# Kernel optimization log

Measured on AMD Instinct MI355X. Metric: run time of the kernel, lower is better.

Reference implementation:

```python
import jax, jax.numpy as jnp
import numpy as np

DIM = 1024
E = 8
K = 2
EPS = 1e-5

def _ln(x, g, b):
    mu = jnp.mean(x, axis=-1, keepdims=True)
    var = jnp.mean(jnp.square(x - mu), axis=-1, keepdims=True)
    return (x - mu) * jax.lax.rsqrt(var + EPS) * g + b

def setup_inputs() -> dict:
    key = jax.random.key(0)
    ks = jax.random.split(key, 8)
    H = 2 * DIM
    s_in = 1.0 / np.sqrt(DIM)
    s_h = 1.0 / np.sqrt(H)
    return {
        "x": jax.random.normal(ks[0], (2, 2048, DIM), dtype=jnp.float32),
        "gate_w": jax.random.uniform(ks[1], (DIM, E), minval=-s_in, maxval=s_in, dtype=jnp.float32),
        "w1": jax.random.uniform(ks[2], (E, DIM, H), minval=-s_in, maxval=s_in, dtype=jnp.float32),
        "b1": jax.random.uniform(ks[3], (E, H), minval=-s_in, maxval=s_in, dtype=jnp.float32),
        "ln1_g": jnp.ones((E, H), dtype=jnp.float32),
        "ln1_b": jnp.zeros((E, H), dtype=jnp.float32),
        "w2": jax.random.uniform(ks[4], (E, H, DIM), minval=-s_h, maxval=s_h, dtype=jnp.float32),
        "b2": jax.random.uniform(ks[5], (E, DIM), minval=-s_h, maxval=s_h, dtype=jnp.float32),
        "ln_g": jnp.ones((DIM,), dtype=jnp.float32),
        "ln_b": jnp.zeros((DIM,), dtype=jnp.float32),
    }

def reference(x, gate_w, w1, b1, ln1_g, ln1_b, w2, b2, ln_g, ln_b):
    shape = x.shape
    xf = x.reshape(-1, shape[-1])                      # [T, D]
    gates = jax.nn.softmax(xf @ gate_w, axis=-1)       # [T, E]
    topw, topi = jax.lax.top_k(gates, K)               # [T, K]
    topw = topw / jnp.sum(topw, axis=-1, keepdims=True)
    # combine weights per expert: [T, E]
    combine = jnp.sum(topw[:, :, None] * jax.nn.one_hot(topi, E, dtype=xf.dtype), axis=1)
    # run all experts on all tokens (vectorized grouped GEMM), combine by gate mask
    h = jnp.einsum('td,edh->teh', xf, w1) + b1          # [T, E, 2D]
    h = _ln(h, ln1_g, ln1_b)
    h = jax.nn.gelu(h, approximate=False)
    y = jnp.einsum('teh,ehd->ted', h, w2) + b2          # [T, E, D]
    out = jnp.einsum('ted,te->td', y, combine)          # [T, D]
    out = _ln(out + xf, ln_g, ln_b)
    return out.reshape(shape)
```

## Files before the change

### kernel.cpp

```cpp
#include <hip/hip_runtime.h>
#include <hip/hip_bf16.h>

#define DIMX 1024
#define HID  2048
#define NE   8
#define NT   4096
#define NPAIR 8192
#define MAXSTRIP 72

typedef __attribute__((ext_vector_type(8))) __bf16 bf16x8;
typedef __attribute__((ext_vector_type(4))) float f32x4;

__device__ inline unsigned short f2bf(float f) {
  union { float f; unsigned u; } v; v.f = f;
  unsigned r = v.u + 0x7FFFu + ((v.u >> 16) & 1u);
  return (unsigned short)(r >> 16);
}
__device__ inline float bf2f(unsigned short h) {
  union { unsigned u; float f; } v; v.u = ((unsigned)h) << 16;
  return v.f;
}

__device__ __forceinline__ void gload_lds16(const unsigned short* g, unsigned short* l) {
  __builtin_amdgcn_global_load_lds(
      (const __attribute__((address_space(1))) unsigned int*)g,
      (__attribute__((address_space(3))) unsigned int*)l, 16, 0, 0);
}

#define O_CNT   0u
#define O_TOK   1024u
#define O_TK    132096u
#define O_PW    263168u
#define O_TI    394240u
#define O_TW    427008u
#define O_POFF  459776u
#define O_SE    459904u
#define O_SR0   460416u
#define O_XBF   524288u
#define O_W1T   16777216u
#define O_W2T   50331648u
#define O_H     83886080u
#define O_Y     121634816u

__global__ __launch_bounds__(256) void k_gate_cvt(const float* __restrict__ x,
                                                  const float* __restrict__ gw,
                                                  unsigned short* __restrict__ xbf,
                                                  int* __restrict__ ti,
                                                  float* __restrict__ tw) {
  int t = blockIdx.x * 4 + (threadIdx.x >> 6);
  int lane = threadIdx.x & 63;
  const float4* xr = (const float4*)(x + (size_t)t * DIMX);
  ushort4* xo = (ushort4*)(xbf + (size_t)t * DIMX);
  float p[NE];
#pragma unroll
  for (int e = 0; e < NE; e++) p[e] = 0.f;
#pragma unroll
  for (int j = 0; j < 4; j++) {
    int idx4 = j * 64 + lane;
    float4 v = xr[idx4];
    ushort4 o; o.x = f2bf(v.x); o.y = f2bf(v.y); o.z = f2bf(v.z); o.w = f2bf(v.w);
    xo[idx4] = o;
    const float4* gp = (const float4*)(gw + (size_t)(idx4 * 4) * NE);
    float4 gA = gp[0], gB = gp[1], gC = gp[2], gD = gp[3];
    float4 gE = gp[4], gF = gp[5], gG = gp[6], gH = gp[7];
    p[0] += v.x * gA.x + v.y * gC.x + v.z * gE.x + v.w * gG.x;
    p[1] += v.x * gA.y + v.y * gC.y + v.z * gE.y + v.w * gG.y;
    p[2] += v.x * gA.z + v.y * gC.z + v.z * gE.z + v.w * gG.z;
    p[3] += v.x * gA.w + v.y * gC.w + v.z * gE.w + v.w * gG.w;
    p[4] += v.x * gB.x + v.y * gD.x + v.z * gF.x + v.w * gH.x;
    p[5] += v.x * gB.y + v.y * gD.y + v.z * gF.y + v.w * gH.y;
    p[6] += v.x * gB.z + v.y * gD.z + v.z * gF.z + v.w * gH.z;
    p[7] += v.x * gB.w + v.y * gD.w + v.z * gF.w + v.w * gH.w;
  }
#pragma unroll
  for (int e = 0; e < NE; e++)
#pragma unroll
    for (int off = 32; off > 0; off >>= 1) p[e] += __shfl_xor(p[e], off);
  if (lane == 0) {
    int ia = 0; float va = p[0];
#pragma unroll
    for (int e = 1; e < NE; e++) if (p[e] > va) { va = p[e]; ia = e; }
    int ib = -1; float vb = -3.0e38f;
#pragma unroll
    for (int e = 0; e < NE; e++) { if (e == ia) continue; if (p[e] > vb) { vb = p[e]; ib = e; } }
    float w0 = 1.f / (1.f + expf(vb - va));
    ti[t * 2] = ia;     tw[t * 2] = w0;
    ti[t * 2 + 1] = ib; tw[t * 2 + 1] = 1.f - w0;
  }
}

__global__ __launch_bounds__(512) void k_build(const int* __restrict__ ti,
                                               const float* __restrict__ tw,
                                               int* __restrict__ cnt,
                                               int* __restrict__ poffs,
                                               int* __restrict__ s_e, int* __restrict__ s_r0,
                                               int* __restrict__ ptok, int* __restrict__ ptk,
                                               float* __restrict__ pw) {
  __shared__ int sti[NPAIR];
  __shared__ int scnt[NE];
  for (int i = threadIdx.x; i < NPAIR; i += 512) sti[i] = ti[i];
  __syncthreads();
  int wid = threadIdx.x >> 6;
  int lane = threadIdx.x & 63;
  int c = 0;
  for (int p = lane; p < NPAIR; p += 64) c += (sti[p] == wid) ? 1 : 0;
#pragma unroll
  for (int off = 32; off > 0; off >>= 1) c += __shfl_xor(c, off);
  if (lane == 0) scnt[wid] = c;
  __syncthreads();
  if (threadIdx.x == 0) {
    int s = 0, pacc = 0;
    for (int e = 0; e < NE; e++) {
      cnt[e] = scnt[e];
      poffs[e] = pacc;
      int ns = (scnt[e] + 127) >> 7;
      for (int k = 0; k < ns; k++) { s_e[s] = e; s_r0[s] = k * 128; s++; }
      pacc += ns * 128;
    }
    poffs[NE] = pacc;
    for (; s < MAXSTRIP; s++) { s_e[s] = -1; s_r0[s] = 0; }
  }
  int base = 0;
  for (int p0 = 0; p0 < NPAIR; p0 += 64) {
    int p = p0 + lane;
    bool m = (sti[p] == wid);
    unsigned long long mask = __ballot(m);
    if (m) {
      int pos = base + __popcll(mask & ((1ull << lane) - 1ull));
      ptok[wid * NT + pos] = p >> 1;
      ptk[wid * NT + pos] = p;
      pw[wid * NT + pos] = tw[p];
    }
    base += __popcll(mask);
  }
}

__global__ __launch_bounds__(256) void k_transpose_cvt(const float* __restrict__ in,
                                                       unsigned short* __restrict__ out,
                                                       int R, int C) {
  __shared__ float tile[64][73];
  int e = blockIdx.z;
  const float* ip = in + (size_t)e * R * C;
  unsigned short* op = out + (size_t)e * R * C;
  int c0 = blockIdx.x * 64, r0 = blockIdx.y * 64;
  int tx = threadIdx.x & 15, ty = threadIdx.x >> 4;
#pragma unroll
  for (int i = 0; i < 4; i++) {
    int row = ty + i * 16;
    float4 v = *(const float4*)(ip + (size_t)(r0 + row) * C + c0 + tx * 4);
    tile[row][tx * 4] = v.x; tile[row][tx * 4 + 1] = v.y;
    tile[row][tx * 4 + 2] = v.z; tile[row][tx * 4 + 3] = v.w;
  }
  __syncthreads();
  int rx = threadIdx.x & 15, cy = threadIdx.x >> 4;
  int r_off = rx * 4;
#pragma unroll
  for (int i = 0; i < 4; i++) {
    int cc = cy + i * 16;
    ushort4 h;
    h.x = f2bf(tile[r_off][cc]);     h.y = f2bf(tile[r_off + 1][cc]);
    h.z = f2bf(tile[r_off + 2][cc]); h.w = f2bf(tile[r_off + 3][cc]);
    *(ushort4*)(op + (size_t)(c0 + cc) * R + r0 + r_off) = h;
  }
}

#define BM 128
#define BN 128
#define BK 32

__global__ __launch_bounds__(256) void k_gemm1(
    const unsigned short* __restrict__ xbf,
    const unsigned short* __restrict__ w1t,
    const float* __restrict__ bias1,
    const int* __restrict__ cnt, const int* __restrict__ s_e,
    const int* __restrict__ s_r0, const int* __restrict__ poffs,
    const int* __restrict__ ptok,
    unsigned short* __restrict__ hpre)
{
  int s = blockIdx.y;
  int e = s_e[s];
  if (e < 0) return;
  int r0e = s_r0[s];
  int n_e = cnt[e];
  int pbase = poffs[e];
  int col0 = blockIdx.x * BN;

  __shared__ __align__(16) unsigned short As[BM][BK];
  __shared__ __align__(16) unsigned short Bs[BN][BK];

  int tid = threadIdx.x;
  int lane = tid & 63, wid = tid >> 6;
  int wr = wid >> 1, wc = wid & 1;
  int quad = lane >> 4, m16 = lane & 15;

  int i4 = lane >> 2, kc = lane & 3;
  int ga0 = r0e + wid * 32 + i4;      if (ga0 >= n_e) ga0 = n_e - 1;
  int ga1 = r0e + wid * 32 + 16 + i4; if (ga1 >= n_e) ga1 = n_e - 1;
  int t0 = ptok[e * NT + ga0];
  int t1 = ptok[e * NT + ga1];
  const unsigned short* a0p = xbf + (size_t)t0 * DIMX + kc * 8;
  const unsigned short* a1p = xbf + (size_t)t1 * DIMX + kc * 8;
  const unsigned short* bb = w1t + (size_t)e * HID * DIMX;
  const unsigned short* b0p = bb + (size_t)(col0 + wid * 32 + i4) * DIMX + kc * 8;
  const unsigned short* b1p = bb + (size_t)(col0 + wid * 32 + 16 + i4) * DIMX + kc * 8;
  unsigned short* lA0 = &As[wid * 32][0];
  unsigned short* lA1 = &As[wid * 32 + 16][0];
  unsigned short* lB0 = &Bs[wid * 32][0];
  unsigned short* lB1 = &Bs[wid * 32 + 16][0];

  f32x4 acc[4][4];
#pragma unroll
  for (int i = 0; i < 4; i++)
#pragma unroll
    for (int j = 0; j < 4; j++) acc[i][j] = (f32x4)(0.f);

  for (int k0 = 0; k0 < DIMX; k0 += BK) {
    __syncthreads();
    gload_lds16(a0p + k0, lA0);
    gload_lds16(a1p + k0, lA1);
    gload_lds16(b0p + k0, lB0);
    gload_lds16(b1p + k0, lB1);
    __syncthreads();
    bf16x8 af[4], bfr[4];
#pragma unroll
    for (int i = 0; i < 4; i++) af[i]  = *(const bf16x8*)&As[wr * 64 + i * 16 + m16][quad * 8];
#pragma unroll
    for (int i = 0; i < 4; i++) bfr[i] = *(const bf16x8*)&Bs[wc * 64 + i * 16 + m16][quad * 8];
#pragma unroll
    for (int i = 0; i < 4; i++)
#pragma unroll
      for (int j = 0; j < 4; j++)
        acc[i][j] = __builtin_amdgcn_mfma_f32_16x16x32_bf16(af[i], bfr[j], acc[i][j], 0, 0, 0);
  }

#pragma unroll
  for (int i = 0; i < 4; i++) {
#pragma unroll
    for (int r = 0; r < 4; r++) {
      int g = r0e + wr * 64 + i * 16 + quad * 4 + r;
      if (g < n_e) {
        size_t rowbase = (size_t)(pbase + g) * HID;
#pragma unroll
        for (int j = 0; j < 4; j++) {
          int colg = col0 + wc * 64 + j * 16 + m16;
          float val = acc[i][j][r] + bias1[e * HID + colg];
          hpre[rowbase + colg] = f2bf(val);
        }
      }
    }
  }
}

__global__ __launch_bounds__(256) void k_ln_gelu(unsigned short* __restrict__ h,
                                                 const float* __restrict__ g1,
                                                 const float* __restrict__ bb1,
                                                 const int* __restrict__ s_e) {
  __shared__ float sbuf[4];
  int row = blockIdx.x;
  int e = s_e[row >> 7];
  if (e < 0) return;
  int tid = threadIdx.x;
  unsigned short* p = h + (size_t)row * HID;
  ushort4 u0 = ((const ushort4*)p)[tid * 2];
  ushort4 u1 = ((const ushort4*)p)[tid * 2 + 1];
  float v[8];
  v[0] = bf2f(u0.x); v[1] = bf2f(u0.y); v[2] = bf2f(u0.z); v[3] = bf2f(u0.w);
  v[4] = bf2f(u1.x); v[5] = bf2f(u1.y); v[6] = bf2f(u1.z); v[7] = bf2f(u1.w);
  float s = 0.f;
#pragma unroll
  for (int i = 0; i < 8; i++) s += v[i];
#pragma unroll
  for (int off = 32; off > 0; off >>= 1) s += __shfl_xor(s, off);
  if ((tid & 63) == 0) sbuf[tid >> 6] = s;
  __syncthreads();
  float mean = (sbuf[0] + sbuf[1] + sbuf[2] + sbuf[3]) * (1.f / HID);
  float sq = 0.f;
#pragma unroll
  for (int i = 0; i < 8; i++) { float d = v[i] - mean; sq += d * d; }
#pragma unroll
  for (int off = 32; off > 0; off >>= 1) sq += __shfl_xor(sq, off);
  __syncthreads();
  if ((tid & 63) == 0) sbuf[tid >> 6] = sq;
  __syncthreads();
  float var = (sbuf[0] + sbuf[1] + sbuf[2] + sbuf[3]) * (1.f / HID);
  float rstd = rsqrtf(var + 1e-5f);
  const float4* gg = (const float4*)(g1 + (size_t)e * HID);
  const float4* gb = (const float4*)(bb1 + (size_t)e * HID);
  float4 ga = gg[tid * 2], gbv = gg[tid * 2 + 1];
  float4 ba = gb[tid * 2], bbv = gb[tid * 2 + 1];
  float gn[8] = {ga.x, ga.y, ga.z, ga.w, gbv.x, gbv.y, gbv.z, gbv.w};
  float bn[8] = {ba.x, ba.y, ba.z, ba.w, bbv.x, bbv.y, bbv.z, bbv.w};
  unsigned short o[8];
#pragma unroll
  for (int i = 0; i < 8; i++) {
    float xn = (v[i] - mean) * rstd * gn[i] + bn[i];
    float ge = 0.5f * xn * (1.f + erff(xn * 0.7071067811865476f));
    o[i] = f2bf(ge);
  }
  ushort4 s0 = {o[0], o[1], o[2], o[3]};
  ushort4 s1 = {o[4], o[5], o[6], o[7]};
  ((ushort4*)p)[tid * 2] = s0;
  ((ushort4*)p)[tid * 2 + 1] = s1;
}

__global__ __launch_bounds__(256) void k_gemm2(
    const unsigned short* __restrict__ hb,
    const unsigned short* __restrict__ w2t,
    const float* __restrict__ bias2,
    const int* __restrict__ cnt, const int* __restrict__ s_e,
    const int* __restrict__ s_r0, const int* __restrict__ poffs,
    const int* __restrict__ ptk, const float* __restrict__ pw,
    float* __restrict__ ybuf)
{
  int s = blockIdx.y;
  int e = s_e[s];
  if (e < 0) return;
  int r0e = s_r0[s];
  int n_e = cnt[e];
  int pbase = poffs[e];
  int col0 = blockIdx.x * BN;

  __shared__ __align__(16) unsigned short As[BM][BK];
  __shared__ __align__(16) unsigned short Bs[BN][BK];

  int tid = threadIdx.x;
  int lane = tid & 63, wid = tid >> 6;
  int wr = wid >> 1, wc = wid & 1;
  int quad = lane >> 4, m16 = lane & 15;

  int i4 = lane >> 2, kc = lane & 3;
  int ga0 = r0e + wid * 32 + i4;      if (ga0 >= n_e) ga0 = n_e - 1;
  int ga1 = r0e + wid * 32 + 16 + i4; if (ga1 >= n_e) ga1 = n_e - 1;
  const unsigned short* a0p = hb + (size_t)(pbase + ga0) * HID + kc * 8;
  const unsigned short* a1p = hb + (size_t)(pbase + ga1) * HID + kc * 8;
  const unsigned short* bb = w2t + (size_t)e * DIMX * HID;
  const unsigned short* b0p = bb + (size_t)(col0 + wid * 32 + i4) * HID + kc * 8;
  const unsigned short* b1p = bb + (size_t)(col0 + wid * 32 + 16 + i4) * HID + kc * 8;
  unsigned short* lA0 = &As[wid * 32][0];
  unsigned short* lA1 = &As[wid * 32 + 16][0];
  unsigned short* lB0 = &Bs[wid * 32][0];
  unsigned short* lB1 = &Bs[wid * 32 + 16][0];

  f32x4 acc[4][4];
#pragma unroll
  for (int i = 0; i < 4; i++)
#pragma unroll
    for (int j = 0; j < 4; j++) acc[i][j] = (f32x4)(0.f);

  for (int k0 = 0; k0 < HID; k0 += BK) {
    __syncthreads();
    gload_lds16(a0p + k0, lA0);
    gload_lds16(a1p + k0, lA1);
    gload_lds16(b0p + k0, lB0);
    gload_lds16(b1p + k0, lB1);
    __syncthreads();
    bf16x8 af[4], bfr[4];
#pragma unroll
    for (int i = 0; i < 4; i++) af[i]  = *(const bf16x8*)&As[wr * 64 + i * 16 + m16][quad * 8];
#pragma unroll
    for (int i = 0; i < 4; i++) bfr[i] = *(const bf16x8*)&Bs[wc * 64 + i * 16 + m16][quad * 8];
#pragma unroll
    for (int i = 0; i < 4; i++)
#pragma unroll
      for (int j = 0; j < 4; j++)
        acc[i][j] = __builtin_amdgcn_mfma_f32_16x16x32_bf16(af[i], bfr[j], acc[i][j], 0, 0, 0);
  }

#pragma unroll
  for (int i = 0; i < 4; i++) {
#pragma unroll
    for (int r = 0; r < 4; r++) {
      int g = r0e + wr * 64 + i * 16 + quad * 4 + r;
      if (g < n_e) {
        int pi = e * NT + g;
        float w = pw[pi];
        size_t obase = (size_t)ptk[pi] * DIMX;
#pragma unroll
        for (int j = 0; j < 4; j++) {
          int colg = col0 + wc * 64 + j * 16 + m16;
          ybuf[obase + colg] = (acc[i][j][r] + bias2[e * DIMX + colg]) * w;
        }
      }
    }
  }
}

__global__ __launch_bounds__(256) void k_final(const float* __restrict__ yb,
                                               const float* __restrict__ x,
                                               const float* __restrict__ lg,
                                               const float* __restrict__ lb,
                                               float* __restrict__ out) {
  __shared__ float sbuf[4];
  int t = blockIdx.x, tid = threadIdx.x;
  const float4* y0 = (const float4*)(yb + (size_t)t * 2 * DIMX);
  const float4* y1 = y0 + DIMX / 4;
  const float4* x4 = (const float4*)(x + (size_t)t * DIMX);
  float4 a = y0[tid], b = y1[tid], c = x4[tid];
  float4 v; v.x = a.x + b.x + c.x; v.y = a.y + b.y + c.y;
  v.z = a.z + b.z + c.z; v.w = a.w + b.w + c.w;
  float s = v.x + v.y + v.z + v.w;
#pragma unroll
  for (int off = 32; off > 0; off >>= 1) s += __shfl_xor(s, off);
  if ((tid & 63) == 0) sbuf[tid >> 6] = s;
  __syncthreads();
  float mean = (sbuf[0] + sbuf[1] + sbuf[2] + sbuf[3]) * (1.f / DIMX);
  float dx = v.x - mean, dy = v.y - mean, dz = v.z - mean, dw = v.w - mean;
  float sq = dx * dx + dy * dy + dz * dz + dw * dw;
#pragma unroll
  for (int off = 32; off > 0; off >>= 1) sq += __shfl_xor(sq, off);
  __syncthreads();
  if ((tid & 63) == 0) sbuf[tid >> 6] = sq;
  __syncthreads();
  float var = (sbuf[0] + sbuf[1] + sbuf[2] + sbuf[3]) * (1.f / DIMX);
  float rstd = rsqrtf(var + 1e-5f);
  float4 g = ((const float4*)lg)[tid], bb = ((const float4*)lb)[tid];
  float4 o; o.x = dx * rstd * g.x + bb.x; o.y = dy * rstd * g.y + bb.y;
  o.z = dz * rstd * g.z + bb.z; o.w = dw * rstd * g.w + bb.w;
  ((float4*)(out + (size_t)t * DIMX))[tid] = o;
}

extern "C" void kernel_launch(void* const* d_in, const int* in_sizes, int n_in,
                              void* d_out, int out_size, void* d_ws, size_t ws_size,
                              hipStream_t stream) {
  const float* x     = (const float*)d_in[0];
  const float* gw    = (const float*)d_in[1];
  const float* w1    = (const float*)d_in[2];
  const float* b1    = (const float*)d_in[3];
  const float* ln1g  = (const float*)d_in[4];
  const float* ln1b  = (const float*)d_in[5];
  const float* w2    = (const float*)d_in[6];
  const float* b2    = (const float*)d_in[7];
  const float* lng   = (const float*)d_in[8];
  const float* lnb   = (const float*)d_in[9];
  float* out = (float*)d_out;

  char* ws = (char*)d_ws;
  int* cnt   = (int*)(ws + O_CNT);
  int* ptok  = (int*)(ws + O_TOK);
  int* ptk   = (int*)(ws + O_TK);
  float* pw  = (float*)(ws + O_PW);
  int* ti    = (int*)(ws + O_TI);
  float* tw  = (float*)(ws + O_TW);
  int* poffs = (int*)(ws + O_POFF);
  int* s_e   = (int*)(ws + O_SE);
  int* s_r0  = (int*)(ws + O_SR0);
  unsigned short* xbf  = (unsigned short*)(ws + O_XBF);
  unsigned short* w1t  = (unsigned short*)(ws + O_W1T);
  unsigned short* w2t  = (unsigned short*)(ws + O_W2T);
  unsigned short* hpre = (unsigned short*)(ws + O_H);
  float* ybuf = (float*)(ws + O_Y);

  hipLaunchKernelGGL(k_gate_cvt, dim3(NT / 4), dim3(256), 0, stream, x, gw, xbf, ti, tw);
  hipLaunchKernelGGL(k_build, dim3(1), dim3(512), 0, stream, ti, tw, cnt, poffs, s_e, s_r0,
                     ptok, ptk, pw);
  hipLaunchKernelGGL(k_transpose_cvt, dim3(HID / 64, DIMX / 64, NE), dim3(256), 0, stream,
                     w1, w1t, DIMX, HID);
  hipLaunchKernelGGL(k_transpose_cvt, dim3(DIMX / 64, HID / 64, NE), dim3(256), 0, stream,
                     w2, w2t, HID, DIMX);
  hipLaunchKernelGGL(k_gemm1, dim3(HID / BN, MAXSTRIP), dim3(256), 0, stream,
                     xbf, w1t, b1, cnt, s_e, s_r0, poffs, ptok, hpre);
  hipLaunchKernelGGL(k_ln_gelu, dim3(MAXSTRIP * BM), dim3(256), 0, stream, hpre, ln1g, ln1b, s_e);
  hipLaunchKernelGGL(k_gemm2, dim3(DIMX / BN, MAXSTRIP), dim3(256), 0, stream,
                     hpre, w2t, b2, cnt, s_e, s_r0, poffs, ptk, pw, ybuf);
  hipLaunchKernelGGL(k_final, dim3(NT), dim3(256), 0, stream, ybuf, x, lng, lnb, out);
}
```

Measured before the change: 401.9 us.

## Double GEMM K-tile to 64 with XOR-swizzled LDS layout and hoisted bias

Both expert GEMMs now use a K tile of 64 instead of 32, which halves the number of barrier-separated load/compute iterations. Global-to-LDS loads place each 16-byte chunk at an XOR-swizzled column so the MFMA fragment reads avoid LDS bank conflicts. Bias values are loaded once per thread before the epilogue instead of inside the store loop, and k_build now stages the gate weights in shared memory. LDS use per block doubles, which may lower occupancy, and the swizzle must match exactly between the stores and the reads.

```diff
diff --git a/kernel.cpp b/kernel.cpp
--- a/kernel.cpp
+++ b/kernel.cpp
@@ -97,8 +97,9 @@
                                                int* __restrict__ ptok, int* __restrict__ ptk,
                                                float* __restrict__ pw) {
   __shared__ int sti[NPAIR];
+  __shared__ float stw[NPAIR];
   __shared__ int scnt[NE];
-  for (int i = threadIdx.x; i < NPAIR; i += 512) sti[i] = ti[i];
+  for (int i = threadIdx.x; i < NPAIR; i += 512) { sti[i] = ti[i]; stw[i] = tw[i]; }
   __syncthreads();
   int wid = threadIdx.x >> 6;
   int lane = threadIdx.x & 63;
@@ -129,7 +130,7 @@
       int pos = base + __popcll(mask & ((1ull << lane) - 1ull));
       ptok[wid * NT + pos] = p >> 1;
       ptk[wid * NT + pos] = p;
-      pw[wid * NT + pos] = tw[p];
+      pw[wid * NT + pos] = stw[p];
     }
     base += __popcll(mask);
   }
@@ -166,7 +167,7 @@
 
 #define BM 128
 #define BN 128
-#define BK 32
+#define BK 64
 
 __global__ __launch_bounds__(256) void k_gemm1(
     const unsigned short* __restrict__ xbf,
@@ -193,20 +194,19 @@
   int wr = wid >> 1, wc = wid & 1;
   int quad = lane >> 4, m16 = lane & 15;
 
-  int i4 = lane >> 2, kc = lane & 3;
-  int ga0 = r0e + wid * 32 + i4;      if (ga0 >= n_e) ga0 = n_e - 1;
-  int ga1 = r0e + wid * 32 + 16 + i4; if (ga1 >= n_e) ga1 = n_e - 1;
-  int t0 = ptok[e * NT + ga0];
-  int t1 = ptok[e * NT + ga1];
-  const unsigned short* a0p = xbf + (size_t)t0 * DIMX + kc * 8;
-  const unsigned short* a1p = xbf + (size_t)t1 * DIMX + kc * 8;
-  const unsigned short* bb = w1t + (size_t)e * HID * DIMX;
-  const unsigned short* b0p = bb + (size_t)(col0 + wid * 32 + i4) * DIMX + kc * 8;
-  const unsigned short* b1p = bb + (size_t)(col0 + wid * 32 + 16 + i4) * DIMX + kc * 8;
-  unsigned short* lA0 = &As[wid * 32][0];
-  unsigned short* lA1 = &As[wid * 32 + 16][0];
-  unsigned short* lB0 = &Bs[wid * 32][0];
-  unsigned short* lB1 = &Bs[wid * 32 + 16][0];
+  int r8 = lane >> 3, c8 = lane & 7;
+  int csrc = (c8 ^ r8) * 8;
+  const unsigned short* aP[4];
+  const unsigned short* bP[4];
+  const unsigned short* bbase = w1t + (size_t)e * HID * DIMX;
+#pragma unroll
+  for (int t = 0; t < 4; t++) {
+    int gr = r0e + wid * 32 + t * 8 + r8; if (gr >= n_e) gr = n_e - 1;
+    int tok = ptok[e * NT + gr];
+    aP[t] = xbf + (size_t)tok * DIMX + csrc;
+    int gc = col0 + wid * 32 + t * 8 + r8;
+    bP[t] = bbase + (size_t)gc * DIMX + csrc;
+  }
 
   f32x4 acc[4][4];
 #pragma unroll
@@ -216,23 +216,30 @@
 
   for (int k0 = 0; k0 < DIMX; k0 += BK) {
     __syncthreads();
-    gload_lds16(a0p + k0, lA0);
-    gload_lds16(a1p + k0, lA1);
-    gload_lds16(b0p + k0, lB0);
-    gload_lds16(b1p + k0, lB1);
+#pragma unroll
+    for (int t = 0; t < 4; t++) gload_lds16(aP[t] + k0, &As[wid * 32 + t * 8][0]);
+#pragma unroll
+    for (int t = 0; t < 4; t++) gload_lds16(bP[t] + k0, &Bs[wid * 32 + t * 8][0]);
     __syncthreads();
-    bf16x8 af[4], bfr[4];
-#pragma unroll
-    for (int i = 0; i < 4; i++) af[i]  = *(const bf16x8*)&As[wr * 64 + i * 16 + m16][quad * 8];
-#pragma unroll
-    for (int i = 0; i < 4; i++) bfr[i] = *(const bf16x8*)&Bs[wc * 64 + i * 16 + m16][quad * 8];
-#pragma unroll
-    for (int i = 0; i < 4; i++)
-#pragma unroll
-      for (int j = 0; j < 4; j++)
-        acc[i][j] = __builtin_amdgcn_mfma_f32_16x16x32_bf16(af[i], bfr[j], acc[i][j], 0, 0, 0);
-  }
-
+#pragma unroll
+    for (int ks = 0; ks < 2; ks++) {
+      int ca = (((quad + 4 * ks) ^ (m16 & 7))) * 8;
+      bf16x8 af[4], bfr[4];
+#pragma unroll
+      for (int i = 0; i < 4; i++) af[i]  = *(const bf16x8*)&As[wr * 64 + i * 16 + m16][ca];
+#pragma unroll
+      for (int j = 0; j < 4; j++) bfr[j] = *(const bf16x8*)&Bs[wc * 64 + j * 16 + m16][ca];
+#pragma unroll
+      for (int i = 0; i < 4; i++)
+#pragma unroll
+        for (int j = 0; j < 4; j++)
+          acc[i][j] = __builtin_amdgcn_mfma_f32_16x16x32_bf16(af[i], bfr[j], acc[i][j], 0, 0, 0);
+    }
+  }
+
+  float bj[4];
+#pragma unroll
+  for (int j = 0; j < 4; j++) bj[j] = bias1[e * HID + col0 + wc * 64 + j * 16 + m16];
 #pragma unroll
   for (int i = 0; i < 4; i++) {
 #pragma unroll
@@ -243,8 +250,7 @@
 #pragma unroll
         for (int j = 0; j < 4; j++) {
           int colg = col0 + wc * 64 + j * 16 + m16;
-          float val = acc[i][j][r] + bias1[e * HID + colg];
-          hpre[rowbase + colg] = f2bf(val);
+          hpre[rowbase + colg] = f2bf(acc[i][j][r] + bj[j]);
         }
       }
     }
@@ -328,18 +334,18 @@
   int wr = wid >> 1, wc = wid & 1;
   int quad = lane >> 4, m16 = lane & 15;
 
-  int i4 = lane >> 2, kc = lane & 3;
-  int ga0 = r0e + wid * 32 + i4;      if (ga0 >= n_e) ga0 = n_e - 1;
-  int ga1 = r0e + wid * 32 + 16 + i4; if (ga1 >= n_e) ga1 = n_e - 1;
-  const unsigned short* a0p = hb + (size_t)(pbase + ga0) * HID + kc * 8;
-  const unsigned short* a1p = hb + (size_t)(pbase + ga1) * HID + kc * 8;
-  const unsigned short* bb = w2t + (size_t)e * DIMX * HID;
-  const unsigned short* b0p = bb + (size_t)(col0 + wid * 32 + i4) * HID + kc * 8;
-  const unsigned short* b1p = bb + (size_t)(col0 + wid * 32 + 16 + i4) * HID + kc * 8;
-  unsigned short* lA0 = &As[wid * 32][0];
-  unsigned short* lA1 = &As[wid * 32 + 16][0];
-  unsigned short* lB0 = &Bs[wid * 32][0];
-  unsigned short* lB1 = &Bs[wid * 32 + 16][0];
+  int r8 = lane >> 3, c8 = lane & 7;
+  int csrc = (c8 ^ r8) * 8;
+  const unsigned short* aP[4];
+  const unsigned short* bP[4];
+  const unsigned short* bbase = w2t + (size_t)e * DIMX * HID;
+#pragma unroll
+  for (int t = 0; t < 4; t++) {
+    int gr = r0e + wid * 32 + t * 8 + r8; if (gr >= n_e) gr = n_e - 1;
+    aP[t] = hb + (size_t)(pbase + gr) * HID + csrc;
+    int gc = col0 + wid * 32 + t * 8 + r8;
+    bP[t] = bbase + (size_t)gc * HID + csrc;
+  }
 
   f32x4 acc[4][4];
 #pragma unroll
@@ -349,23 +355,30 @@
 
   for (int k0 = 0; k0 < HID; k0 += BK) {
     __syncthreads();
-    gload_lds16(a0p + k0, lA0);
-    gload_lds16(a1p + k0, lA1);
-    gload_lds16(b0p + k0, lB0);
-    gload_lds16(b1p + k0, lB1);
+#pragma unroll
+    for (int t = 0; t < 4; t++) gload_lds16(aP[t] + k0, &As[wid * 32 + t * 8][0]);
+#pragma unroll
+    for (int t = 0; t < 4; t++) gload_lds16(bP[t] + k0, &Bs[wid * 32 + t * 8][0]);
     __syncthreads();
-    bf16x8 af[4], bfr[4];
-#pragma unroll
-    for (int i = 0; i < 4; i++) af[i]  = *(const bf16x8*)&As[wr * 64 + i * 16 + m16][quad * 8];
-#pragma unroll
-    for (int i = 0; i < 4; i++) bfr[i] = *(const bf16x8*)&Bs[wc * 64 + i * 16 + m16][quad * 8];
-#pragma unroll
-    for (int i = 0; i < 4; i++)
-#pragma unroll
-      for (int j = 0; j < 4; j++)
-        acc[i][j] = __builtin_amdgcn_mfma_f32_16x16x32_bf16(af[i], bfr[j], acc[i][j], 0, 0, 0);
-  }
-
+#pragma unroll
+    for (int ks = 0; ks < 2; ks++) {
+      int ca = (((quad + 4 * ks) ^ (m16 & 7))) * 8;
+      bf16x8 af[4], bfr[4];
+#pragma unroll
+      for (int i = 0; i < 4; i++) af[i]  = *(const bf16x8*)&As[wr * 64 + i * 16 + m16][ca];
+#pragma unroll
+      for (int j = 0; j < 4; j++) bfr[j] = *(const bf16x8*)&Bs[wc * 64 + j * 16 + m16][ca];
+#pragma unroll
+      for (int i = 0; i < 4; i++)
+#pragma unroll
+        for (int j = 0; j < 4; j++)
+          acc[i][j] = __builtin_amdgcn_mfma_f32_16x16x32_bf16(af[i], bfr[j], acc[i][j], 0, 0, 0);
+    }
+  }
+
+  float bj[4];
+#pragma unroll
+  for (int j = 0; j < 4; j++) bj[j] = bias2[e * DIMX + col0 + wc * 64 + j * 16 + m16];
 #pragma unroll
   for (int i = 0; i < 4; i++) {
 #pragma unroll
@@ -378,7 +391,7 @@
 #pragma unroll
         for (int j = 0; j < 4; j++) {
           int colg = col0 + wc * 64 + j * 16 + m16;
-          ybuf[obase + colg] = (acc[i][j][r] + bias2[e * DIMX + colg]) * w;
+          ybuf[obase + colg] = (acc[i][j][r] + bj[j]) * w;
         }
       }
     }
```

After: 391.2 us. 1.03x faster.
